# Optimization experiments

Hardware: AMD Instinct MI355X
Metric: run time of the kernel (lower is better)

The kernel has to match this reference:

```python
import jax, jax.numpy as jnp
import numpy as np

DIM = 2048
DIM_SEQ = 2048
DIM_OUT = DIM // 2
LN_EPS = 1e-5


def setup_inputs() -> dict:
    key = jax.random.key(0)
    k1, k2 = jax.random.split(key)
    x = jax.random.normal(k1, (8, DIM_SEQ, DIM), dtype=jnp.float32)
    init_eps = 0.001 / DIM_SEQ
    # Conv1d(dim_seq, dim_seq, 1) weight -> [seq, seq] seq-mixing matrix
    proj_w = jax.random.uniform(k2, (DIM_SEQ, DIM_SEQ), minval=-init_eps, maxval=init_eps, dtype=jnp.float32)
    proj_b = jnp.ones((DIM_SEQ,), dtype=jnp.float32)
    ln_scale = jnp.ones((DIM_OUT,), dtype=jnp.float32)
    ln_bias = jnp.zeros((DIM_OUT,), dtype=jnp.float32)
    return {"x": x, "proj_w": proj_w, "proj_b": proj_b, "ln_scale": ln_scale, "ln_bias": ln_bias}


def reference(x, proj_w, proj_b, ln_scale, ln_bias):
    # chunk into residual and gate halves along feature dim
    res, gate = jnp.split(x, 2, axis=-1)  # each [b, s, d/2]
    # LayerNorm over last dim of gate
    mu = jnp.mean(gate, axis=-1, keepdims=True)
    var = jnp.mean(jnp.square(gate - mu), axis=-1, keepdims=True)
    gate = (gate - mu) * jax.lax.rsqrt(var + LN_EPS) * ln_scale + ln_bias
    # Conv1d kernel=1 over seq axis == seq-mixing matmul: [s,t] x [b,t,d] -> [b,s,d]
    gate = jnp.einsum('st,btd->bsd', proj_w, gate) + proj_b[None, :, None]
    # act = Identity; gated residual multiply
    return gate * res
```

## Files before the change

kernel.cpp:

```cpp
#include <hip/hip_runtime.h>

typedef __attribute__((ext_vector_type(8))) short short8;
typedef __attribute__((ext_vector_type(4))) float floatx4;

__device__ __forceinline__ unsigned short f2bf(float f) {
    unsigned int u = __builtin_bit_cast(unsigned int, f);
    u += 0x7fffu + ((u >> 16) & 1u);
    return (unsigned short)(u >> 16);
}

__device__ __forceinline__ void async16(unsigned short* lds, const unsigned short* g) {
    __builtin_amdgcn_global_load_lds(
        (__attribute__((address_space(1))) void*)(g),
        (__attribute__((address_space(3))) void*)(lds),
        16, 0, 0);
}

#define DIM      2048
#define DSEQ     2048
#define DOUT     1024
#define NBATCH   8
#define NBCHUNK  4
#define NCHUNK   (NBATCH / NBCHUNK)
#define NKB      (DSEQ / 32)


__global__ __launch_bounds__(256) void cast_w_kernel(const float* __restrict__ w,
                                                     unsigned short* __restrict__ o) {
    int i = (blockIdx.x * 256 + threadIdx.x) * 4;
    int s = i >> 11;
    int t = i & 2047;
    float4 v = *(const float4*)(w + i);
    unsigned int lo = (unsigned int)f2bf(v.x) | ((unsigned int)f2bf(v.y) << 16);
    unsigned int hi = (unsigned int)f2bf(v.z) | ((unsigned int)f2bf(v.w) << 16);
    unsigned short* dst = o + (((size_t)(t >> 5)) * DSEQ + s) * 32 + (t & 31);
    *(uint2*)dst = make_uint2(lo, hi);
}

__global__ __launch_bounds__(256) void ln_t_kernel(const float* __restrict__ X,
                                                   const float* __restrict__ lns,
                                                   const float* __restrict__ lnb,
                                                   unsigned short* __restrict__ Gt) {
    const int tid  = threadIdx.x;
    const int wave = tid >> 6;
    const int lane = tid & 63;
    const int t0   = blockIdx.x * 32;
    const int b    = blockIdx.y;

    __shared__ unsigned short lt[32][1028];

    float4 sc[4], bi[4];
    #pragma unroll
    for (int c = 0; c < 4; ++c) {
        sc[c] = *(const float4*)(lns + c * 256 + lane * 4);
        bi[c] = *(const float4*)(lnb + c * 256 + lane * 4);
    }

    #pragma unroll 1
    for (int i = 0; i < 8; ++i) {
        const int r = wave * 8 + i;
        const float* xr = X + ((size_t)(b * DSEQ + t0 + r)) * DIM + DOUT;
        float4 v[4];
        float s = 0.f, ss = 0.f;
        #pragma unroll
        for (int c = 0; c < 4; ++c) {
            v[c] = *(const float4*)(xr + c * 256 + lane * 4);
            s  += v[c].x + v[c].y + v[c].z + v[c].w;
            ss += v[c].x * v[c].x + v[c].y * v[c].y + v[c].z * v[c].z + v[c].w * v[c].w;
        }
        #pragma unroll
        for (int off = 32; off > 0; off >>= 1) {
            s  += __shfl_xor(s,  off, 64);
            ss += __shfl_xor(ss, off, 64);
        }
        const float mu  = s * (1.f / 1024.f);
        const float var = ss * (1.f / 1024.f) - mu * mu;
        const float inv = rsqrtf(var + 1e-5f);
        #pragma unroll
        for (int c = 0; c < 4; ++c) {
            const int d = c * 256 + lane * 4;
            float y0 = (v[c].x - mu) * inv * sc[c].x + bi[c].x;
            float y1 = (v[c].y - mu) * inv * sc[c].y + bi[c].y;
            float y2 = (v[c].z - mu) * inv * sc[c].z + bi[c].z;
            float y3 = (v[c].w - mu) * inv * sc[c].w + bi[c].w;
            unsigned int lo = (unsigned int)f2bf(y0) | ((unsigned int)f2bf(y1) << 16);
            unsigned int hi = (unsigned int)f2bf(y2) | ((unsigned int)f2bf(y3) << 16);
            *(uint2*)&lt[r][d] = make_uint2(lo, hi);
        }
    }
    __syncthreads();

    #pragma unroll
    for (int it = 0; it < 4; ++it) {
        const int d = it * 256 + tid;
        unsigned int u[16];
        #pragma unroll
        for (int j = 0; j < 16; ++j)
            u[j] = (unsigned int)lt[2 * j][d] | ((unsigned int)lt[2 * j + 1][d] << 16);
        uint4* dst = (uint4*)(Gt + (((size_t)b * NKB + (t0 >> 5)) * DOUT + d) * 32);
        dst[0] = make_uint4(u[0],  u[1],  u[2],  u[3]);
        dst[1] = make_uint4(u[4],  u[5],  u[6],  u[7]);
        dst[2] = make_uint4(u[8],  u[9],  u[10], u[11]);
        dst[3] = make_uint4(u[12], u[13], u[14], u[15]);
    }
}

#define BM 128
#define BN 128

__global__ __launch_bounds__(256) void gemm_sgu(const unsigned short* __restrict__ Wt,
                                                const unsigned short* __restrict__ Gt,
                                                const float* __restrict__ X,
                                                const float* __restrict__ Pb,
                                                float* __restrict__ Out) {
    const int tid = threadIdx.x;
    const int s0  = blockIdx.x * BM;
    const int d0  = blockIdx.y * BN;
    const int b   = blockIdx.z;

    __shared__ __align__(16) unsigned char smem[32768];

    const int wave = tid >> 6;
    const int lane = tid & 63;
    const int wr   = wave >> 1;
    const int wc   = wave & 1;
    const int ln15 = lane & 15;
    const int q    = lane >> 4;

    int ldsOff[2], srcA[2], srcB[2];
    #pragma unroll
    for (int j = 0; j < 2; ++j) {
        const int c  = tid + j * 256;
        const int r  = c >> 2;
        const int kc = (c & 3) ^ (r & 3);
        ldsOff[j] = c * 8;
        srcA[j]   = (s0 + r) * 32 + kc * 8;
        srcB[j]   = (d0 + r) * 32 + kc * 8;
    }
    int aOff[4], bOff[4];
    #pragma unroll
    for (int i = 0; i < 4; ++i) {
        const int ra = wr * 64 + i * 16 + ln15;
        const int rb = wc * 64 + i * 16 + ln15;
        aOff[i] = ra * 32 + ((q ^ (ra & 3)) * 8);
        bOff[i] = rb * 32 + ((q ^ (rb & 3)) * 8);
    }

    floatx4 acc[4][4] = {};

    const unsigned short* gB = Gt + (size_t)b * NKB * DOUT * 32;

    {
        const unsigned short* aBase = Wt;
        const unsigned short* bBase = gB;
        unsigned short* As = (unsigned short*)(smem);
        unsigned short* Bs = (unsigned short*)(smem + 8192);
        #pragma unroll
        for (int j = 0; j < 2; ++j) {
            async16(&As[ldsOff[j]], aBase + srcA[j]);
            async16(&Bs[ldsOff[j]], bBase + srcB[j]);
        }
    }

    for (int kb = 0; kb < NKB; ++kb) {
        unsigned short* Asc = (unsigned short*)(smem + (kb & 1) * 16384);
        unsigned short* Bsc = Asc + 8192 / 2;
        __syncthreads();

        if (kb + 1 < NKB) {
            const unsigned short* aBase = Wt + (size_t)(kb + 1) * DSEQ * 32;
            const unsigned short* bBase = gB + (size_t)(kb + 1) * DOUT * 32;
            unsigned short* Asn = (unsigned short*)(smem + ((kb + 1) & 1) * 16384);
            unsigned short* Bsn = Asn + 8192 / 2;
            #pragma unroll
            for (int j = 0; j < 2; ++j) {
                async16(&Asn[ldsOff[j]], aBase + srcA[j]);
                async16(&Bsn[ldsOff[j]], bBase + srcB[j]);
            }
        }

        short8 af[4], bf[4];
        #pragma unroll
        for (int i = 0; i < 4; ++i) af[i] = *(const short8*)&Asc[aOff[i]];
        #pragma unroll
        for (int i = 0; i < 4; ++i) bf[i] = *(const short8*)&Bsc[bOff[i]];
        #pragma unroll
        for (int i = 0; i < 4; ++i)
            #pragma unroll
            for (int j = 0; j < 4; ++j)
                acc[i][j] = __builtin_amdgcn_mfma_f32_16x16x32_bf16(af[i], bf[j], acc[i][j], 0, 0, 0);
    }

    float (*ep)[132] = (float (*)[132])smem;
    const int gr  = tid >> 3;
    const int seg = tid & 7;
    #pragma unroll
    for (int e = 0; e < 4; ++e) {
        __syncthreads();
        #pragma unroll
        for (int j = 0; j < 4; ++j) {
            const int C = wc * 64 + j * 16 + ln15;
            #pragma unroll
            for (int r = 0; r < 4; ++r)
                ep[wr * 16 + q * 4 + r][C] = acc[e][j][r];
        }
        __syncthreads();
        const int s = s0 + (gr >> 4) * 64 + e * 16 + (gr & 15);
        const int d = d0 + seg * 16;
        const float pb = Pb[s];
        const float* xr = X + ((size_t)(b * DSEQ + s)) * DIM + d;
        float*       orow = Out + ((size_t)(b * DSEQ + s)) * DOUT + d;
        #pragma unroll
        for (int w = 0; w < 4; ++w) {
            float4 c = *(const float4*)&ep[gr][seg * 16 + w * 4];
            float4 x = *(const float4*)(xr + w * 4);
            float4 o;
            o.x = (c.x + pb) * x.x;
            o.y = (c.y + pb) * x.y;
            o.z = (c.z + pb) * x.z;
            o.w = (c.w + pb) * x.w;
            *(float4*)(orow + w * 4) = o;
        }
    }
}

extern "C" void kernel_launch(void* const* d_in, const int* in_sizes, int n_in,
                              void* d_out, int out_size, void* d_ws, size_t ws_size,
                              hipStream_t stream) {
    const float* x    = (const float*)d_in[0];
    const float* pw   = (const float*)d_in[1];
    const float* pb   = (const float*)d_in[2];
    const float* lns  = (const float*)d_in[3];
    const float* lnb  = (const float*)d_in[4];
    float* out        = (float*)d_out;

    unsigned short* Wt = (unsigned short*)d_ws;
    unsigned short* Gt = (unsigned short*)((char*)d_ws + (size_t)DSEQ * DSEQ * 2);

    cast_w_kernel<<<dim3((DSEQ * DSEQ) / 1024), dim3(256), 0, stream>>>(pw, Wt);

    const size_t xChunk = (size_t)NBCHUNK * DSEQ * DIM;
    const size_t oChunk = (size_t)NBCHUNK * DSEQ * DOUT;
    for (int c = 0; c < NCHUNK; ++c) {
        ln_t_kernel<<<dim3(DSEQ / 32, NBCHUNK), dim3(256), 0, stream>>>(
            x + c * xChunk, lns, lnb, Gt);
        gemm_sgu<<<dim3(DSEQ / BM, DOUT / BN, NBCHUNK), dim3(256), 0, stream>>>(
            Wt, Gt, x + c * xChunk, pb, out + c * oChunk);
    }
}
```

Before: 325.9 us.

## Double K-step per barrier in SGU GEMM and remap block indices

Result: faster. 318.6 us (-2.2%).

```diff
diff --git a/kernel.cpp b/kernel.cpp
--- a/kernel.cpp
+++ b/kernel.cpp
@@ -23,6 +23,7 @@
 #define NBCHUNK  4
 #define NCHUNK   (NBATCH / NBCHUNK)
 #define NKB      (DSEQ / 32)
+#define NKT      (NKB / 2)
 
 
 __global__ __launch_bounds__(256) void cast_w_kernel(const float* __restrict__ w,
@@ -114,11 +115,13 @@
                                                 const float* __restrict__ Pb,
                                                 float* __restrict__ Out) {
     const int tid = threadIdx.x;
-    const int s0  = blockIdx.x * BM;
-    const int d0  = blockIdx.y * BN;
+    const int ys  = blockIdx.x & 7;
+    const int xs  = (blockIdx.x >> 3) | (blockIdx.y << 1);
+    const int s0  = xs * BM;
+    const int d0  = ys * BN;
     const int b   = blockIdx.z;
 
-    __shared__ __align__(16) unsigned char smem[32768];
+    __shared__ __align__(16) unsigned char smem[65536];
 
     const int wave = tid >> 6;
     const int lane = tid & 63;
@@ -151,44 +154,60 @@
     const unsigned short* gB = Gt + (size_t)b * NKB * DOUT * 32;
 
     {
-        const unsigned short* aBase = Wt;
-        const unsigned short* bBase = gB;
         unsigned short* As = (unsigned short*)(smem);
-        unsigned short* Bs = (unsigned short*)(smem + 8192);
+        unsigned short* Bs = As + 8192;
         #pragma unroll
         for (int j = 0; j < 2; ++j) {
-            async16(&As[ldsOff[j]], aBase + srcA[j]);
-            async16(&Bs[ldsOff[j]], bBase + srcB[j]);
-        }
-    }
-
-    for (int kb = 0; kb < NKB; ++kb) {
-        unsigned short* Asc = (unsigned short*)(smem + (kb & 1) * 16384);
-        unsigned short* Bsc = Asc + 8192 / 2;
+            async16(As + ldsOff[j],        Wt + srcA[j]);
+            async16(As + 4096 + ldsOff[j], Wt + (size_t)DSEQ * 32 + srcA[j]);
+            async16(Bs + ldsOff[j],        gB + srcB[j]);
+            async16(Bs + 4096 + ldsOff[j], gB + (size_t)DOUT * 32 + srcB[j]);
+        }
+    }
+
+    for (int t = 0; t < NKT; ++t) {
+        unsigned short* Ab = (unsigned short*)(smem + (t & 1) * 32768);
+        unsigned short* Bb = Ab + 8192;
         __syncthreads();
 
-        if (kb + 1 < NKB) {
-            const unsigned short* aBase = Wt + (size_t)(kb + 1) * DSEQ * 32;
-            const unsigned short* bBase = gB + (size_t)(kb + 1) * DOUT * 32;
-            unsigned short* Asn = (unsigned short*)(smem + ((kb + 1) & 1) * 16384);
-            unsigned short* Bsn = Asn + 8192 / 2;
+        if (t + 1 < NKT) {
+            const unsigned short* aB0 = Wt + (size_t)(2 * t + 2) * (DSEQ * 32);
+            const unsigned short* bB0 = gB + (size_t)(2 * t + 2) * (DOUT * 32);
+            unsigned short* An = (unsigned short*)(smem + ((t + 1) & 1) * 32768);
+            unsigned short* Bn = An + 8192;
             #pragma unroll
             for (int j = 0; j < 2; ++j) {
-                async16(&Asn[ldsOff[j]], aBase + srcA[j]);
-                async16(&Bsn[ldsOff[j]], bBase + srcB[j]);
+                async16(An + ldsOff[j],        aB0 + srcA[j]);
+                async16(An + 4096 + ldsOff[j], aB0 + DSEQ * 32 + srcA[j]);
+                async16(Bn + ldsOff[j],        bB0 + srcB[j]);
+                async16(Bn + 4096 + ldsOff[j], bB0 + DOUT * 32 + srcB[j]);
             }
         }
 
-        short8 af[4], bf[4];
-        #pragma unroll
-        for (int i = 0; i < 4; ++i) af[i] = *(const short8*)&Asc[aOff[i]];
-        #pragma unroll
-        for (int i = 0; i < 4; ++i) bf[i] = *(const short8*)&Bsc[bOff[i]];
-        #pragma unroll
-        for (int i = 0; i < 4; ++i)
-            #pragma unroll
-            for (int j = 0; j < 4; ++j)
-                acc[i][j] = __builtin_amdgcn_mfma_f32_16x16x32_bf16(af[i], bf[j], acc[i][j], 0, 0, 0);
+        {
+            short8 af[4], bf[4];
+            #pragma unroll
+            for (int i = 0; i < 4; ++i) af[i] = *(const short8*)&Ab[aOff[i]];
+            #pragma unroll
+            for (int i = 0; i < 4; ++i) bf[i] = *(const short8*)&Bb[bOff[i]];
+            #pragma unroll
+            for (int i = 0; i < 4; ++i)
+                #pragma unroll
+                for (int j = 0; j < 4; ++j)
+                    acc[i][j] = __builtin_amdgcn_mfma_f32_16x16x32_bf16(af[i], bf[j], acc[i][j], 0, 0, 0);
+        }
+        {
+            short8 af[4], bf[4];
+            #pragma unroll
+            for (int i = 0; i < 4; ++i) af[i] = *(const short8*)&Ab[4096 + aOff[i]];
+            #pragma unroll
+            for (int i = 0; i < 4; ++i) bf[i] = *(const short8*)&Bb[4096 + bOff[i]];
+            #pragma unroll
+            for (int i = 0; i < 4; ++i)
+                #pragma unroll
+                for (int j = 0; j < 4; ++j)
+                    acc[i][j] = __builtin_amdgcn_mfma_f32_16x16x32_bf16(af[i], bf[j], acc[i][j], 0, 0, 0);
+        }
     }
 
     float (*ep)[132] = (float (*)[132])smem;
@@ -244,7 +263,7 @@
     for (int c = 0; c < NCHUNK; ++c) {
         ln_t_kernel<<<dim3(DSEQ / 32, NBCHUNK), dim3(256), 0, stream>>>(
             x + c * xChunk, lns, lnb, Gt);
-        gemm_sgu<<<dim3(DSEQ / BM, DOUT / BN, NBCHUNK), dim3(256), 0, stream>>>(
+        gemm_sgu<<<dim3(16, 8, NBCHUNK), dim3(256), 0, stream>>>(
             Wt, Gt, x + c * xChunk, pb, out + c * oChunk);
     }
 }
```
